# Kernel optimization log

Measured on AMD Instinct MI355X. Metric: run time of the kernel, lower is better.

## Reference

```python
import jax, jax.numpy as jnp
import numpy as np


def setup_inputs() -> dict:
    key = jax.random.key(0)
    k1, k2 = jax.random.split(key)
    pc1 = jax.random.normal(k1, (8, 2048, 3), dtype=jnp.float32)
    pc2 = jax.random.normal(k2, (8, 2048, 3), dtype=jnp.float32)
    return {"pc1": pc1, "pc2": pc2}


def reference(pc1, pc2):
    # Flatten to point lists, matching pc.reshape(-1, 3)
    p1 = pc1.reshape(-1, 3)  # [N1, 3]
    p2 = pc2.reshape(-1, 3)  # [N2, 3]
    # Squared pairwise distances via ||a||^2 + ||b||^2 - 2 a.b
    sq1 = jnp.sum(p1 * p1, axis=-1)  # [N1]
    sq2 = jnp.sum(p2 * p2, axis=-1)  # [N2]
    d2 = sq1[:, None] + sq2[None, :] - 2.0 * jnp.einsum('nd,md->nm', p1, p2)  # [N1, N2]
    d2 = jnp.maximum(d2, 0.0)
    d = jnp.sqrt(d2)  # Euclidean, matching cKDTree.query distances
    # dist1 = NN distance from each pc2 point into pc1 (tree1.query(pc2))
    dist1 = jnp.min(d, axis=0)  # [N2]
    # dist2 = NN distance from each pc1 point into pc2 (tree2.query(pc1))
    dist2 = jnp.min(d, axis=1)  # [N1]
    return jnp.mean(dist1) + jnp.mean(dist2)
```

## Files before the change

### kernel.cpp

```cpp
#include <hip/hip_runtime.h>
#include <math.h>

#define N_PTS 16384
#define TPB   256
#define IP    4
#define IBLK  (N_PTS / (TPB * IP))
#define JT    512
#define JS    (N_PTS / JT)
#define REDB  64

__global__ __launch_bounds__(TPB) void chamfer_pack(
    const float* __restrict__ p1, const float* __restrict__ p2,
    float4* __restrict__ P, unsigned int* __restrict__ dmin,
    float* __restrict__ outp) {
  int id = blockIdx.x * TPB + threadIdx.x;
  const float* src = (id < N_PTS) ? p1 : p2;
  int k = (id < N_PTS) ? id : (id - N_PTS);
  float x = src[3 * k + 0], y = src[3 * k + 1], z = src[3 * k + 2];
  P[id] = make_float4(x, y, z, 0.5f * (x * x + y * y + z * z));
  dmin[id] = 0x7F800000u;
  if (id == 0) outp[0] = 0.f;
}

__global__ __launch_bounds__(TPB) void chamfer_min(
    const float4* __restrict__ P, unsigned int* __restrict__ dmin) {
  __shared__ float4 tile[JT];
  const int dir = blockIdx.z;
  const float4* __restrict__ Q = P + (size_t)dir * N_PTS;
  const float4* __restrict__ T = P + (size_t)(1 - dir) * N_PTS;
  unsigned int* __restrict__ out = dmin + (size_t)dir * N_PTS;

  const int jbase = blockIdx.x * JT;
  for (int t = threadIdx.x; t < JT; t += TPB)
    tile[t] = T[jbase + t];
  __syncthreads();

  const int i0 = blockIdx.y * (TPB * IP) + threadIdx.x * IP;
  float nx[IP], ny[IP], nz[IP], cw[IP], vmin[IP];
#pragma unroll
  for (int k = 0; k < IP; ++k) {
    float4 p = Q[i0 + k];
    nx[k] = -p.x; ny[k] = -p.y; nz[k] = -p.z; cw[k] = p.w;
    vmin[k] = INFINITY;
  }

#pragma unroll 8
  for (int j = 0; j < JT; j += 2) {
    float4 qa = tile[j];
    float4 qb = tile[j + 1];
#pragma unroll
    for (int k = 0; k < IP; ++k) {
      float va = fmaf(nx[k], qa.x, qa.w);
      va = fmaf(ny[k], qa.y, va);
      va = fmaf(nz[k], qa.z, va);
      float vb = fmaf(nx[k], qb.x, qb.w);
      vb = fmaf(ny[k], qb.y, vb);
      vb = fmaf(nz[k], qb.z, vb);
      asm("v_min3_f32 %0, %1, %2, %3"
          : "=v"(vmin[k]) : "v"(va), "v"(vb), "v"(vmin[k]));
    }
  }

#pragma unroll
  for (int k = 0; k < IP; ++k) {
    float d2 = fmaxf(0.f, 2.f * (cw[k] + vmin[k]));
    atomicMin(&out[i0 + k], __float_as_uint(d2));
  }
}

__global__ __launch_bounds__(TPB) void chamfer_reduce(
    const unsigned int* __restrict__ dmin, float* __restrict__ outp) {
  float s = 0.f;
  for (int i = blockIdx.x * TPB + threadIdx.x; i < 2 * N_PTS; i += REDB * TPB)
    s += sqrtf(__uint_as_float(dmin[i]));
#pragma unroll
  for (int off = 32; off > 0; off >>= 1)
    s += __shfl_down(s, off, 64);
  __shared__ float partial[TPB / 64];
  if ((threadIdx.x & 63) == 0) partial[threadIdx.x >> 6] = s;
  __syncthreads();
  if (threadIdx.x == 0) {
    float t = 0.f;
    for (int w = 0; w < TPB / 64; ++w) t += partial[w];
    atomicAdd(outp, t * (1.0f / (float)N_PTS));
  }
}

extern "C" void kernel_launch(void* const* d_in, const int* in_sizes, int n_in,
                              void* d_out, int out_size, void* d_ws, size_t ws_size,
                              hipStream_t stream) {
  const float* pc1 = (const float*)d_in[0];
  const float* pc2 = (const float*)d_in[1];
  float4* P = (float4*)d_ws;
  unsigned int* dmin = (unsigned int*)((char*)d_ws + (size_t)2 * N_PTS * sizeof(float4));
  float* outp = (float*)d_out;

  chamfer_pack<<<(2 * N_PTS) / TPB, TPB, 0, stream>>>(pc1, pc2, P, dmin, outp);
  chamfer_min<<<dim3(JS, IBLK, 2), TPB, 0, stream>>>(P, dmin);
  chamfer_reduce<<<REDB, TPB, 0, stream>>>(dmin, outp);
}
```

Baseline: 99.91 us.

## Fuse pack, min and reduce into one cooperative kernel with grid syncs

Merges the three kernels into a single cooperative launch: dmin is initialised, a grid sync follows, the min pass runs, then another grid sync and the sqrt/sum reduction. Each block now builds its own tile from the raw xyz inputs and computes the half-norms on the fly, so the packed float4 buffer and its global round trip are gone. IP is doubled to 8 points per thread, which halves the grid to 512 blocks (with launch_bounds 2). This saves two launches and the intermediate buffer traffic. In exchange it adds grid-wide barriers, has fewer blocks to spread across the CUs, and raises register pressure.

```diff
diff --git a/kernel.cpp b/kernel.cpp
--- a/kernel.cpp
+++ b/kernel.cpp
@@ -1,47 +1,62 @@
 #include <hip/hip_runtime.h>
+#include <hip/hip_cooperative_groups.h>
 #include <math.h>
+
+namespace cg = cooperative_groups;
 
 #define N_PTS 16384
 #define TPB   256
-#define IP    4
+#define IP    8
 #define IBLK  (N_PTS / (TPB * IP))
 #define JT    512
 #define JS    (N_PTS / JT)
-#define REDB  64
+#define GRID  (JS * IBLK * 2)
 
-__global__ __launch_bounds__(TPB) void chamfer_pack(
+__global__ __launch_bounds__(TPB, 2) void chamfer_fused(
     const float* __restrict__ p1, const float* __restrict__ p2,
-    float4* __restrict__ P, unsigned int* __restrict__ dmin,
-    float* __restrict__ outp) {
-  int id = blockIdx.x * TPB + threadIdx.x;
-  const float* src = (id < N_PTS) ? p1 : p2;
-  int k = (id < N_PTS) ? id : (id - N_PTS);
-  float x = src[3 * k + 0], y = src[3 * k + 1], z = src[3 * k + 2];
-  P[id] = make_float4(x, y, z, 0.5f * (x * x + y * y + z * z));
-  dmin[id] = 0x7F800000u;
-  if (id == 0) outp[0] = 0.f;
-}
+    unsigned int* __restrict__ dmin, float* __restrict__ outp) {
+  cg::grid_group grid = cg::this_grid();
+  __shared__ float4 tile[JT];
+  const int bid = blockIdx.x;
+  const int tid = threadIdx.x;
 
-__global__ __launch_bounds__(TPB) void chamfer_min(
-    const float4* __restrict__ P, unsigned int* __restrict__ dmin) {
-  __shared__ float4 tile[JT];
-  const int dir = blockIdx.z;
-  const float4* __restrict__ Q = P + (size_t)dir * N_PTS;
-  const float4* __restrict__ T = P + (size_t)(1 - dir) * N_PTS;
-  unsigned int* __restrict__ out = dmin + (size_t)dir * N_PTS;
+  {
+    const int per = 2 * N_PTS / GRID;
+    if (tid < per) dmin[bid * per + tid] = 0x7F7F7F7Fu;
+    if (bid == 0 && tid == 0) atomicExch(outp, 0.0f);
+  }
+  grid.sync();
 
-  const int jbase = blockIdx.x * JT;
-  for (int t = threadIdx.x; t < JT; t += TPB)
-    tile[t] = T[jbase + t];
+  const int js  = bid & (JS - 1);
+  const int ib  = (bid >> 5) & (IBLK - 1);
+  const int dir = bid >> 8;
+  const float* __restrict__ Qraw = dir ? p2 : p1;
+  const float* __restrict__ Traw = dir ? p1 : p2;
+
+  const int jbase = js * JT;
+  for (int t = tid; t < JT; t += TPB) {
+    float x = Traw[3 * (jbase + t) + 0];
+    float y = Traw[3 * (jbase + t) + 1];
+    float z = Traw[3 * (jbase + t) + 2];
+    tile[t] = make_float4(x, y, z, 0.5f * (x * x + y * y + z * z));
+  }
   __syncthreads();
 
-  const int i0 = blockIdx.y * (TPB * IP) + threadIdx.x * IP;
+  const int i0 = ib * (TPB * IP) + tid * IP;
+  float f[24];
+  const float4* __restrict__ Qv = (const float4*)(Qraw + 3 * i0);
+#pragma unroll
+  for (int t = 0; t < 6; ++t) {
+    float4 v = Qv[t];
+    f[4 * t] = v.x; f[4 * t + 1] = v.y; f[4 * t + 2] = v.z; f[4 * t + 3] = v.w;
+  }
   float nx[IP], ny[IP], nz[IP], cw[IP], vmin[IP];
 #pragma unroll
   for (int k = 0; k < IP; ++k) {
-    float4 p = Q[i0 + k];
-    nx[k] = -p.x; ny[k] = -p.y; nz[k] = -p.z; cw[k] = p.w;
-    vmin[k] = INFINITY;
+    float x = f[3 * k], y = f[3 * k + 1], z = f[3 * k + 2];
+    nx[k] = -x; ny[k] = -y; nz[k] = -z;
+    cw[k] = 0.5f * (x * x + y * y + z * z);
+    vmin[k] = 3.0e38f;
   }
 
 #pragma unroll 8
@@ -56,33 +71,25 @@
       float vb = fmaf(nx[k], qb.x, qb.w);
       vb = fmaf(ny[k], qb.y, vb);
       vb = fmaf(nz[k], qb.z, vb);
-      asm("v_min3_f32 %0, %1, %2, %3"
-          : "=v"(vmin[k]) : "v"(va), "v"(vb), "v"(vmin[k]));
+      asm("v_min3_f32 %0, %1, %2, %0" : "+v"(vmin[k]) : "v"(va), "v"(vb));
     }
   }
 
+  unsigned int* __restrict__ out = dmin + (size_t)dir * N_PTS;
 #pragma unroll
   for (int k = 0; k < IP; ++k) {
     float d2 = fmaxf(0.f, 2.f * (cw[k] + vmin[k]));
     atomicMin(&out[i0 + k], __float_as_uint(d2));
   }
-}
+  grid.sync();
 
-__global__ __launch_bounds__(TPB) void chamfer_reduce(
-    const unsigned int* __restrict__ dmin, float* __restrict__ outp) {
-  float s = 0.f;
-  for (int i = blockIdx.x * TPB + threadIdx.x; i < 2 * N_PTS; i += REDB * TPB)
-    s += sqrtf(__uint_as_float(dmin[i]));
+  if (tid < 64) {
+    float s = sqrtf(__uint_as_float(dmin[bid * 64 + tid]));
 #pragma unroll
-  for (int off = 32; off > 0; off >>= 1)
-    s += __shfl_down(s, off, 64);
-  __shared__ float partial[TPB / 64];
-  if ((threadIdx.x & 63) == 0) partial[threadIdx.x >> 6] = s;
-  __syncthreads();
-  if (threadIdx.x == 0) {
-    float t = 0.f;
-    for (int w = 0; w < TPB / 64; ++w) t += partial[w];
-    atomicAdd(outp, t * (1.0f / (float)N_PTS));
+    for (int off = 32; off > 0; off >>= 1)
+      s += __shfl_down(s, off, 64);
+    if (tid == 0)
+      atomicAdd(outp, s * (1.0f / (float)N_PTS));
   }
 }
 
@@ -91,11 +98,10 @@
                               hipStream_t stream) {
   const float* pc1 = (const float*)d_in[0];
   const float* pc2 = (const float*)d_in[1];
-  float4* P = (float4*)d_ws;
-  unsigned int* dmin = (unsigned int*)((char*)d_ws + (size_t)2 * N_PTS * sizeof(float4));
+  unsigned int* dmin = (unsigned int*)d_ws;
   float* outp = (float*)d_out;
 
-  chamfer_pack<<<(2 * N_PTS) / TPB, TPB, 0, stream>>>(pc1, pc2, P, dmin, outp);
-  chamfer_min<<<dim3(JS, IBLK, 2), TPB, 0, stream>>>(P, dmin);
-  chamfer_reduce<<<REDB, TPB, 0, stream>>>(dmin, outp);
+  void* args[] = {(void*)&pc1, (void*)&pc2, (void*)&dmin, (void*)&outp};
+  hipLaunchCooperativeKernel((void*)chamfer_fused, dim3(GRID), dim3(TPB),
+                             args, 0, stream);
 }
```

Result: slower. 216.9 us (+117.1%).
